# Performance work log

Measured on AMD Instinct MI355X. Metric: run time of the kernel, lower is better.

The kernel has to match this reference:

```python
import jax, jax.numpy as jnp
import numpy as np

N = 64      # pmu_number (nodes per graph)
F = 128     # features per PMU chunk
T = 8192    # time steps (graphs in the batch)
H = 128     # encoder hidden
O = 128     # gcn output
E = 512     # edges (fixed topology shared by all time steps)


def setup_inputs() -> dict:
    key = jax.random.key(0)
    ks = jax.random.split(key, 5)
    x = jax.random.normal(ks[0], (T, N * F), dtype=jnp.float32)
    src = jax.random.randint(ks[1], (E,), 0, N, dtype=jnp.int32)
    dst = jax.random.randint(ks[2], (E,), 0, N, dtype=jnp.int32)
    W_enc = jax.random.normal(ks[3], (F, H), dtype=jnp.float32) / np.float32(np.sqrt(F))
    b_enc = jnp.zeros((H,), jnp.float32)
    W_gcn = jax.random.normal(ks[4], (H, O), dtype=jnp.float32) / np.float32(np.sqrt(H))
    b_gcn = jnp.zeros((O,), jnp.float32)
    return {"x": x, "W_enc": W_enc, "b_enc": b_enc, "W_gcn": W_gcn,
            "b_gcn": b_gcn, "src": src, "dst": dst}


def _norm_adj(src, dst, n):
    # dgl.graph((src,dst)) + add_self_loop, GraphConv norm='both':
    # A_hat[i,j] = multiplicity of edge j->i (+ self loop); out = D_in^-1/2 A_hat D_out^-1/2
    A = jnp.zeros((n, n), jnp.float32).at[dst, src].add(1.0)
    A = A + jnp.eye(n, dtype=jnp.float32)
    deg_out = A.sum(axis=0)  # out-degree of source node j
    deg_in = A.sum(axis=1)   # in-degree of destination node i
    return A * jax.lax.rsqrt(deg_in)[:, None] * jax.lax.rsqrt(deg_out)[None, :]


def reference(x, W_enc, b_enc, W_gcn, b_gcn, src, dst):
    # np.split along last axis: chunk i = x[:, i*F:(i+1)*F] -> reshape gives [T, N, F]
    h = x.reshape(T, N, F) @ W_enc + b_enc            # encoder per PMU: [T, N, H]
    norm = _norm_adj(src, dst, N)                      # fixed topology shared across all T graphs
    agg = jnp.einsum('ij,tjh->tih', norm, h)           # batched GCN aggregation
    out = agg @ W_gcn + b_gcn                          # [T, N, O]
    # dgl.batch node ordering: graph 0 nodes, graph 1 nodes, ... -> time-major flatten
    return out.reshape(T * N, O)
```

## Files before the change

kernel.cpp:

```cpp
#include <hip/hip_runtime.h>
#include <hip/hip_bf16.h>

#define T_STEPS 8192
#define NN 64
#define FF 128
#define HH 128
#define OO 128
#define TPB_T 8

typedef _Float16 f16;
typedef __attribute__((ext_vector_type(8))) _Float16 f16x8;
typedef __attribute__((ext_vector_type(4))) _Float16 f16x4;
typedef __attribute__((ext_vector_type(4))) float f32x4;

#define XH_PITCH 136
#define H2_PITCH 72
#define NM_PITCH 72

__global__ void prep_norm_kernel(const int* __restrict__ src, const int* __restrict__ dst, int E,
                                 const float* __restrict__ benc, const float* __restrict__ wgcn,
                                 f16* __restrict__ normg, float* __restrict__ bcg)
{
    __shared__ float A[NN * NN];
    __shared__ float din[NN], dout[NN];
    const int tid = threadIdx.x;
    for (int i = tid; i < NN * NN; i += 256) A[i] = 0.0f;
    __syncthreads();
    for (int e = tid; e < E; e += 256) atomicAdd(&A[dst[e] * NN + src[e]], 1.0f);
    __syncthreads();
    if (tid < NN) A[tid * NN + tid] += 1.0f;
    __syncthreads();
    if (tid < NN) {
        float s = 0.f;
        for (int j = 0; j < NN; ++j) s += A[tid * NN + j];
        din[tid] = s;
    } else if (tid < 2 * NN) {
        int j = tid - NN;
        float s = 0.f;
        for (int i = 0; i < NN; ++i) s += A[i * NN + j];
        dout[j] = s;
    }
    __syncthreads();
    if (tid < NN) {
        float ri = rsqrtf(din[tid]);
        for (int j = 0; j < NN; ++j)
            normg[tid * NN + j] = (f16)(A[tid * NN + j] * ri * rsqrtf(dout[j]));
    }
    if (tid >= 128) {
        int o = tid - 128;
        float s = 0.f;
        for (int h = 0; h < HH; ++h) s += benc[h] * wgcn[h * OO + o];
        bcg[o] = s;
    }
}

__global__ void prep_wc_kernel(const float* __restrict__ wenc, const float* __restrict__ wgcn,
                               f16* __restrict__ wctg)
{
    int o = blockIdx.x * 2 + (threadIdx.x >> 7);
    int f = threadIdx.x & 127;
    float s = 0.f;
    for (int h = 0; h < HH; ++h) s += wenc[f * HH + h] * wgcn[h * OO + o];
    wctg[o * FF + f] = (f16)s;
}

__global__ __launch_bounds__(256, 2) void fused_kernel(
    const float* __restrict__ x, const f16* __restrict__ normg,
    const f16* __restrict__ wctg, const float* __restrict__ bcg,
    const float* __restrict__ bgcn, float* __restrict__ out)
{
    __shared__ f16 xh[NN * XH_PITCH];
    __shared__ f16 h2t[OO * H2_PITCH];
    __shared__ f16 nsh[NN * NM_PITCH];

    const int tid = threadIdx.x;
    const int lane = tid & 63;
    const int w = tid >> 6;
    const int l15 = lane & 15;
    const int lg = lane >> 4;

    for (int c = tid; c < (NN * NN) / 8; c += 256) {
        int row = c >> 3, cb = (c & 7) * 8;
        *(f16x8*)(nsh + row * NM_PITCH + cb) = *(const f16x8*)(normg + row * NN + cb);
    }

    f16x8 wcf[2][4];
#pragma unroll
    for (int ct = 0; ct < 2; ++ct)
#pragma unroll
        for (int kk = 0; kk < 4; ++kk)
            wcf[ct][kk] = *(const f16x8*)(wctg + (w * 32 + ct * 16 + l15) * FF + kk * 32 + lg * 8);

    f32x4 bcs[2];
#pragma unroll
    for (int ct = 0; ct < 2; ++ct) {
        float v = bcg[w * 32 + ct * 16 + l15];
        bcs[ct][0] = v; bcs[ct][1] = v; bcs[ct][2] = v; bcs[ct][3] = v;
    }
    f32x4 bgf[2];
#pragma unroll
    for (int ct = 0; ct < 2; ++ct)
        bgf[ct] = *(const f32x4*)(bgcn + w * 32 + ct * 16 + lg * 4);

    const int t0 = blockIdx.x * TPB_T;

    float4 raA[8], raB[8];
    {
        const float4* xp0 = (const float4*)(x + (size_t)t0 * (NN * FF));
        const float4* xp1 = xp0 + (NN * FF) / 4;
#pragma unroll
        for (int ii = 0; ii < 4; ++ii) {
            int c = tid + 256 * ii;
            raA[2 * ii]     = xp0[2 * c];
            raA[2 * ii + 1] = xp0[2 * c + 1];
        }
#pragma unroll
        for (int ii = 0; ii < 4; ++ii) {
            int c = tid + 256 * ii;
            raB[2 * ii]     = xp1[2 * c];
            raB[2 * ii + 1] = xp1[2 * c + 1];
        }
    }

    auto body = [&](float4 (&rau)[8], int i) {
        const int t = t0 + i;

#pragma unroll
        for (int ii = 0; ii < 4; ++ii) {
            int c = tid + 256 * ii;
            int row = c >> 4, k0 = (c & 15) * 8;
            float4 a = rau[2 * ii], b = rau[2 * ii + 1];
            f16x8 v;
            v[0] = (f16)a.x; v[1] = (f16)a.y; v[2] = (f16)a.z; v[3] = (f16)a.w;
            v[4] = (f16)b.x; v[5] = (f16)b.y; v[6] = (f16)b.z; v[7] = (f16)b.w;
            *(f16x8*)(xh + row * XH_PITCH + k0) = v;
        }
        __syncthreads();

        if (i + 2 < TPB_T) {
            const float4* xq = (const float4*)(x + (size_t)(t + 2) * (NN * FF));
#pragma unroll
            for (int ii = 0; ii < 4; ++ii) {
                int c = tid + 256 * ii;
                rau[2 * ii]     = xq[2 * c];
                rau[2 * ii + 1] = xq[2 * c + 1];
            }
        }

        f32x4 acc1[4][2];
#pragma unroll
        for (int rt = 0; rt < 4; ++rt)
#pragma unroll
            for (int ct = 0; ct < 2; ++ct)
                acc1[rt][ct] = bcs[ct];
#pragma unroll
        for (int kk = 0; kk < 4; ++kk) {
            f16x8 af[4];
#pragma unroll
            for (int rt = 0; rt < 4; ++rt)
                af[rt] = *(const f16x8*)(xh + (rt * 16 + l15) * XH_PITCH + kk * 32 + lg * 8);
#pragma unroll
            for (int rt = 0; rt < 4; ++rt)
#pragma unroll
                for (int ct = 0; ct < 2; ++ct)
                    acc1[rt][ct] = __builtin_amdgcn_mfma_f32_16x16x32_f16(
                        af[rt], wcf[ct][kk], acc1[rt][ct], 0, 0, 0);
        }
        __syncthreads();

#pragma unroll
        for (int rt = 0; rt < 4; ++rt)
#pragma unroll
            for (int ct = 0; ct < 2; ++ct) {
                f16x4 hv;
#pragma unroll
                for (int r = 0; r < 4; ++r) hv[r] = (f16)acc1[rt][ct][r];
                *(f16x4*)(h2t + (w * 32 + ct * 16 + l15) * H2_PITCH + rt * 16 + lg * 4) = hv;
            }

        f32x4 acc2[2][4];
#pragma unroll
        for (int ct = 0; ct < 2; ++ct)
#pragma unroll
            for (int rt = 0; rt < 4; ++rt)
                acc2[ct][rt] = bgf[ct];
#pragma unroll
        for (int kk = 0; kk < 2; ++kk) {
            f16x8 bf[2];
#pragma unroll
            for (int ct = 0; ct < 2; ++ct)
                bf[ct] = *(const f16x8*)(h2t + (w * 32 + ct * 16 + l15) * H2_PITCH + kk * 32 + lg * 8);
            f16x8 nl[4];
#pragma unroll
            for (int rt = 0; rt < 4; ++rt)
                nl[rt] = *(const f16x8*)(nsh + (rt * 16 + l15) * NM_PITCH + kk * 32 + lg * 8);
#pragma unroll
            for (int ct = 0; ct < 2; ++ct)
#pragma unroll
                for (int rt = 0; rt < 4; ++rt)
                    acc2[ct][rt] = __builtin_amdgcn_mfma_f32_16x16x32_f16(
                        bf[ct], nl[rt], acc2[ct][rt], 0, 0, 0);
        }

        float* op = out + (size_t)t * (NN * OO);
#pragma unroll
        for (int rt = 0; rt < 4; ++rt)
#pragma unroll
            for (int ct = 0; ct < 2; ++ct)
                *(f32x4*)(op + (rt * 16 + l15) * OO + w * 32 + ct * 16 + lg * 4) = acc2[ct][rt];
    };

#pragma unroll 1
    for (int i = 0; i < TPB_T; i += 2) {
        body(raA, i);
        body(raB, i + 1);
    }
}

extern "C" void kernel_launch(void* const* d_in, const int* in_sizes, int n_in,
                              void* d_out, int out_size, void* d_ws, size_t ws_size,
                              hipStream_t stream)
{
    const float* x    = (const float*)d_in[0];
    const float* wenc = (const float*)d_in[1];
    const float* benc = (const float*)d_in[2];
    const float* wgcn = (const float*)d_in[3];
    const float* bgcn = (const float*)d_in[4];
    const int*   src  = (const int*)d_in[5];
    const int*   dst  = (const int*)d_in[6];
    const int E = in_sizes[5];

    f16*   wctg  = (f16*)d_ws;
    f16*   normg = (f16*)((char*)d_ws + 32768);
    float* bcg   = (float*)((char*)d_ws + 32768 + 8192);

    prep_norm_kernel<<<1, 256, 0, stream>>>(src, dst, E, benc, wgcn, normg, bcg);
    prep_wc_kernel<<<OO / 2, 256, 0, stream>>>(wenc, wgcn, wctg);
    fused_kernel<<<T_STEPS / TPB_T, 256, 0, stream>>>(x, normg, wctg, bcg, bgcn, (float*)d_out);
}
```

Baseline: 130.2 us.

## Stage x via direct global-to-LDS DMA with swizzled double-buffered fp32 tiles

Replaces the register-staged fp32 loads of x (convert to fp16, then store to padded LDS) with global_load_lds DMA into two fp32 LDS buffers using an XOR swizzle. The fp16 conversion moves to the MFMA operand read. The normalized adjacency fragments now live in registers instead of LDS, and the h2t buffer uses an XOR swizzle instead of padding. One __syncthreads per step goes away, replaced by explicit vmcnt waits and s_barrier. The goal is to cut VGPR pressure and the LDS store pass so the memory stream overlaps better with compute. The cost is much more LDS (two 32KB fp32 buffers), which could limit occupancy, and the design depends on hand-counted vmcnt values.

Result: no change. 131.3 us (+0.8%).

```diff
diff --git a/kernel.cpp b/kernel.cpp
--- a/kernel.cpp
+++ b/kernel.cpp
@@ -1,5 +1,6 @@
 #include <hip/hip_runtime.h>
 #include <hip/hip_bf16.h>
+#include <stdint.h>
 
 #define T_STEPS 8192
 #define NN 64
@@ -12,10 +13,6 @@
 typedef __attribute__((ext_vector_type(8))) _Float16 f16x8;
 typedef __attribute__((ext_vector_type(4))) _Float16 f16x4;
 typedef __attribute__((ext_vector_type(4))) float f32x4;
-
-#define XH_PITCH 136
-#define H2_PITCH 72
-#define NM_PITCH 72
 
 __global__ void prep_norm_kernel(const int* __restrict__ src, const int* __restrict__ dst, int E,
                                  const float* __restrict__ benc, const float* __restrict__ wgcn,
@@ -64,14 +61,20 @@
     wctg[o * FF + f] = (f16)s;
 }
 
+__device__ __forceinline__ void dma16(const float* g, float* l) {
+    __builtin_amdgcn_global_load_lds(
+        (const __attribute__((address_space(1))) uint32_t*)g,
+        (__attribute__((address_space(3))) uint32_t*)l, 16, 0, 0);
+}
+
 __global__ __launch_bounds__(256, 2) void fused_kernel(
     const float* __restrict__ x, const f16* __restrict__ normg,
     const f16* __restrict__ wctg, const float* __restrict__ bcg,
     const float* __restrict__ bgcn, float* __restrict__ out)
 {
-    __shared__ f16 xh[NN * XH_PITCH];
-    __shared__ f16 h2t[OO * H2_PITCH];
-    __shared__ f16 nsh[NN * NM_PITCH];
+    __shared__ float xb0[NN * FF];
+    __shared__ float xb1[NN * FF];
+    __shared__ f16 h2t[OO * NN];
 
     const int tid = threadIdx.x;
     const int lane = tid & 63;
@@ -79,17 +82,19 @@
     const int l15 = lane & 15;
     const int lg = lane >> 4;
 
-    for (int c = tid; c < (NN * NN) / 8; c += 256) {
-        int row = c >> 3, cb = (c & 7) * 8;
-        *(f16x8*)(nsh + row * NM_PITCH + cb) = *(const f16x8*)(normg + row * NN + cb);
-    }
-
     f16x8 wcf[2][4];
 #pragma unroll
     for (int ct = 0; ct < 2; ++ct)
 #pragma unroll
         for (int kk = 0; kk < 4; ++kk)
             wcf[ct][kk] = *(const f16x8*)(wctg + (w * 32 + ct * 16 + l15) * FF + kk * 32 + lg * 8);
+
+    f16x8 nf[4][2];
+#pragma unroll
+    for (int rt = 0; rt < 4; ++rt)
+#pragma unroll
+        for (int kk = 0; kk < 2; ++kk)
+            nf[rt][kk] = *(const f16x8*)(normg + (rt * 16 + l15) * NN + kk * 32 + lg * 8);
 
     f32x4 bcs[2];
 #pragma unroll
@@ -104,49 +109,17 @@
 
     const int t0 = blockIdx.x * TPB_T;
 
-    float4 raA[8], raB[8];
-    {
-        const float4* xp0 = (const float4*)(x + (size_t)t0 * (NN * FF));
-        const float4* xp1 = xp0 + (NN * FF) / 4;
-#pragma unroll
-        for (int ii = 0; ii < 4; ++ii) {
-            int c = tid + 256 * ii;
-            raA[2 * ii]     = xp0[2 * c];
-            raA[2 * ii + 1] = xp0[2 * c + 1];
-        }
-#pragma unroll
-        for (int ii = 0; ii < 4; ++ii) {
-            int c = tid + 256 * ii;
-            raB[2 * ii]     = xp1[2 * c];
-            raB[2 * ii + 1] = xp1[2 * c + 1];
-        }
-    }
-
-    auto body = [&](float4 (&rau)[8], int i) {
-        const int t = t0 + i;
-
-#pragma unroll
-        for (int ii = 0; ii < 4; ++ii) {
-            int c = tid + 256 * ii;
-            int row = c >> 4, k0 = (c & 15) * 8;
-            float4 a = rau[2 * ii], b = rau[2 * ii + 1];
-            f16x8 v;
-            v[0] = (f16)a.x; v[1] = (f16)a.y; v[2] = (f16)a.z; v[3] = (f16)a.w;
-            v[4] = (f16)b.x; v[5] = (f16)b.y; v[6] = (f16)b.z; v[7] = (f16)b.w;
-            *(f16x8*)(xh + row * XH_PITCH + k0) = v;
-        }
-        __syncthreads();
-
-        if (i + 2 < TPB_T) {
-            const float4* xq = (const float4*)(x + (size_t)(t + 2) * (NN * FF));
-#pragma unroll
-            for (int ii = 0; ii < 4; ++ii) {
-                int c = tid + 256 * ii;
-                rau[2 * ii]     = xq[2 * c];
-                rau[2 * ii + 1] = xq[2 * c + 1];
-            }
-        }
-
+    auto stage_x = [&](const float* xt, float* dst) {
+#pragma unroll
+        for (int j = 0; j < 8; ++j) {
+            int c = w * 8 + j;
+            int row = c * 2 + (lane >> 5);
+            int slot = (lane & 31) ^ (row & 7);
+            dma16(xt + row * FF + slot * 4, dst + c * 256);
+        }
+    };
+
+    auto compute = [&](const float* cur, int t) {
         f32x4 acc1[4][2];
 #pragma unroll
         for (int rt = 0; rt < 4; ++rt)
@@ -157,8 +130,17 @@
         for (int kk = 0; kk < 4; ++kk) {
             f16x8 af[4];
 #pragma unroll
-            for (int rt = 0; rt < 4; ++rt)
-                af[rt] = *(const f16x8*)(xh + (rt * 16 + l15) * XH_PITCH + kk * 32 + lg * 8);
+            for (int rt = 0; rt < 4; ++rt) {
+                int row = rt * 16 + l15;
+                int sw = (row & 7) << 2;
+                int d0 = kk * 32 + lg * 8;
+                f32x4 a0 = *(const f32x4*)(cur + row * FF + (d0 ^ sw));
+                f32x4 a1 = *(const f32x4*)(cur + row * FF + ((d0 + 4) ^ sw));
+                f16x8 v;
+                v[0] = (f16)a0[0]; v[1] = (f16)a0[1]; v[2] = (f16)a0[2]; v[3] = (f16)a0[3];
+                v[4] = (f16)a1[0]; v[5] = (f16)a1[1]; v[6] = (f16)a1[2]; v[7] = (f16)a1[3];
+                af[rt] = v;
+            }
 #pragma unroll
             for (int rt = 0; rt < 4; ++rt)
 #pragma unroll
@@ -166,7 +148,6 @@
                     acc1[rt][ct] = __builtin_amdgcn_mfma_f32_16x16x32_f16(
                         af[rt], wcf[ct][kk], acc1[rt][ct], 0, 0, 0);
         }
-        __syncthreads();
 
 #pragma unroll
         for (int rt = 0; rt < 4; ++rt)
@@ -175,7 +156,9 @@
                 f16x4 hv;
 #pragma unroll
                 for (int r = 0; r < 4; ++r) hv[r] = (f16)acc1[rt][ct][r];
-                *(f16x4*)(h2t + (w * 32 + ct * 16 + l15) * H2_PITCH + rt * 16 + lg * 4) = hv;
+                int col = w * 32 + ct * 16 + l15;
+                int idx = (col * 64 + rt * 16 + lg * 4) ^ ((col & 7) << 3);
+                *(f16x4*)(h2t + idx) = hv;
             }
 
         f32x4 acc2[2][4];
@@ -188,18 +171,17 @@
         for (int kk = 0; kk < 2; ++kk) {
             f16x8 bf[2];
 #pragma unroll
-            for (int ct = 0; ct < 2; ++ct)
-                bf[ct] = *(const f16x8*)(h2t + (w * 32 + ct * 16 + l15) * H2_PITCH + kk * 32 + lg * 8);
-            f16x8 nl[4];
-#pragma unroll
-            for (int rt = 0; rt < 4; ++rt)
-                nl[rt] = *(const f16x8*)(nsh + (rt * 16 + l15) * NM_PITCH + kk * 32 + lg * 8);
+            for (int ct = 0; ct < 2; ++ct) {
+                int col = w * 32 + ct * 16 + l15;
+                int idx = (col * 64 + kk * 32 + lg * 8) ^ ((col & 7) << 3);
+                bf[ct] = *(const f16x8*)(h2t + idx);
+            }
 #pragma unroll
             for (int ct = 0; ct < 2; ++ct)
 #pragma unroll
                 for (int rt = 0; rt < 4; ++rt)
                     acc2[ct][rt] = __builtin_amdgcn_mfma_f32_16x16x32_f16(
-                        bf[ct], nl[rt], acc2[ct][rt], 0, 0, 0);
+                        bf[ct], nf[rt][kk], acc2[ct][rt], 0, 0, 0);
         }
 
         float* op = out + (size_t)t * (NN * OO);
@@ -210,10 +192,34 @@
                 *(f32x4*)(op + (rt * 16 + l15) * OO + w * 32 + ct * 16 + lg * 4) = acc2[ct][rt];
     };
 
+    stage_x(x + (size_t)t0 * (NN * FF), xb0);
+    __builtin_amdgcn_sched_barrier(0);
+    asm volatile("s_waitcnt vmcnt(0)");
+    __builtin_amdgcn_sched_barrier(0);
+    __builtin_amdgcn_s_barrier();
+    __builtin_amdgcn_sched_barrier(0);
+
 #pragma unroll 1
     for (int i = 0; i < TPB_T; i += 2) {
-        body(raA, i);
-        body(raB, i + 1);
+        stage_x(x + (size_t)(t0 + i + 1) * (NN * FF), xb1);
+        __builtin_amdgcn_sched_barrier(0);
+        compute(xb0, t0 + i);
+        __builtin_amdgcn_sched_barrier(0);
+        asm volatile("s_waitcnt vmcnt(8)");
+        __builtin_amdgcn_sched_barrier(0);
+        __builtin_amdgcn_s_barrier();
+        __builtin_amdgcn_sched_barrier(0);
+
+        if (i + 2 < TPB_T) stage_x(x + (size_t)(t0 + i + 2) * (NN * FF), xb0);
+        __builtin_amdgcn_sched_barrier(0);
+        compute(xb1, t0 + i + 1);
+        if (i + 2 < TPB_T) {
+            __builtin_amdgcn_sched_barrier(0);
+            asm volatile("s_waitcnt vmcnt(8)");
+            __builtin_amdgcn_sched_barrier(0);
+            __builtin_amdgcn_s_barrier();
+            __builtin_amdgcn_sched_barrier(0);
+        }
     }
 }
 
```
